# Performance work log

Measured on AMD Instinct MI355X. Metric: run time of the kernel, lower is better.

The kernel has to match this reference:

```python
import jax, jax.numpy as jnp
import numpy as np

SEQ, B, I, H = 2048, 64, 512, 512


def setup_inputs() -> dict:
    key = jax.random.key(0)
    ks = jax.random.split(key, 5)
    s = 1.0 / np.sqrt(H)  # torch.nn.RNN init scale
    return {
        "x": jax.random.normal(ks[0], (SEQ, B, I), dtype=jnp.float32),
        "W_ih": jax.random.normal(ks[1], (H, I), dtype=jnp.float32) * s,
        "W_hh": jax.random.normal(ks[2], (H, H), dtype=jnp.float32) * s,
        "b_ih": jax.random.normal(ks[3], (H,), dtype=jnp.float32) * s,
        "b_hh": jax.random.normal(ks[4], (H,), dtype=jnp.float32) * s,
    }


def reference(x, W_ih, W_hh, b_ih, b_hh):
    # Precompute input projection for all timesteps in one big GEMM: [T,B,H]
    xw = jnp.einsum("tbi,hi->tbh", x, W_ih) + b_ih + b_hh

    def step(h, xt):
        # h: [B,H]; xt: [B,H] (already includes x_t W_ih^T + biases)
        h = jnp.tanh(xt + h @ W_hh.T)
        return h, h

    h0 = jnp.zeros((x.shape[1], W_hh.shape[0]), dtype=x.dtype)
    _, out = jax.lax.scan(step, h0, xw)  # out: [T,B,H]
    return out.reshape(-1, W_hh.shape[0])  # [T*B, H], matches out.view(-1, hidden)
```

## Files before the change

### kernel.cpp

```cpp
#include <hip/hip_runtime.h>
#include <cmath>


#define SEQ_T 2048
#define BATCH 64
#define KDIM 512
#define HDIM 512

typedef __fp16 h2v __attribute__((ext_vector_type(2)));
typedef __fp16 f16x8 __attribute__((ext_vector_type(8)));
typedef float f32x4 __attribute__((ext_vector_type(4)));

static __device__ __forceinline__ f16x8 pk8(float4 a, float4 b) {
  h2v p0 = __builtin_amdgcn_cvt_pkrtz(a.x, a.y);
  h2v p1 = __builtin_amdgcn_cvt_pkrtz(a.z, a.w);
  h2v p2 = __builtin_amdgcn_cvt_pkrtz(b.x, b.y);
  h2v p3 = __builtin_amdgcn_cvt_pkrtz(b.z, b.w);
  f16x8 r;
  r[0] = p0[0]; r[1] = p0[1]; r[2] = p1[0]; r[3] = p1[1];
  r[4] = p2[0]; r[5] = p2[1]; r[6] = p3[0]; r[7] = p3[1];
  return r;
}

#define BM 128
#define BN 64
#define BK 32
#define LDA_T (BM + 4)
#define LDB_T (BN + 4)

__global__ __launch_bounds__(256) void xw_gemm(const float* __restrict__ x,
                                               const float* __restrict__ Wih,
                                               const float* __restrict__ bih,
                                               const float* __restrict__ bhh,
                                               float* __restrict__ out) {
  __shared__ float As[BK * LDA_T];
  __shared__ float Bs[BK * LDB_T];
  const int tid = threadIdx.x;
  const int nb = blockIdx.x & 7;
  const int mb = blockIdx.x >> 3;
  const int m0 = mb * BM;
  const int n0 = nb * BN;
  const int tx = tid & 15;
  const int ty = tid >> 4;

  float acc[8][4];
#pragma unroll
  for (int i = 0; i < 8; ++i)
#pragma unroll
    for (int j = 0; j < 4; ++j) acc[i][j] = 0.f;

  for (int k0 = 0; k0 < KDIM; k0 += BK) {
#pragma unroll
    for (int p = 0; p < 4; ++p) {
      int idx = tid + p * 256;
      int r = idx >> 3, c = idx & 7;
      float4 a = *(const float4*)(x + (size_t)(m0 + r) * KDIM + k0 + c * 4);
      As[(c * 4 + 0) * LDA_T + r] = a.x;
      As[(c * 4 + 1) * LDA_T + r] = a.y;
      As[(c * 4 + 2) * LDA_T + r] = a.z;
      As[(c * 4 + 3) * LDA_T + r] = a.w;
    }
#pragma unroll
    for (int p = 0; p < 2; ++p) {
      int idx = tid + p * 256;
      int r = idx >> 3, c = idx & 7;
      float4 bv = *(const float4*)(Wih + (size_t)(n0 + r) * KDIM + k0 + c * 4);
      Bs[(c * 4 + 0) * LDB_T + r] = bv.x;
      Bs[(c * 4 + 1) * LDB_T + r] = bv.y;
      Bs[(c * 4 + 2) * LDB_T + r] = bv.z;
      Bs[(c * 4 + 3) * LDB_T + r] = bv.w;
    }
    __syncthreads();
#pragma unroll
    for (int kk = 0; kk < BK; ++kk) {
      float4 a0 = *(const float4*)(As + kk * LDA_T + ty * 8);
      float4 a1 = *(const float4*)(As + kk * LDA_T + ty * 8 + 4);
      float4 b0 = *(const float4*)(Bs + kk * LDB_T + tx * 4);
      float am[8] = {a0.x, a0.y, a0.z, a0.w, a1.x, a1.y, a1.z, a1.w};
      float bn_[4] = {b0.x, b0.y, b0.z, b0.w};
#pragma unroll
      for (int i = 0; i < 8; ++i)
#pragma unroll
        for (int j = 0; j < 4; ++j) acc[i][j] = fmaf(am[i], bn_[j], acc[i][j]);
    }
    __syncthreads();
  }

  float4 bi = *(const float4*)(bih + n0 + tx * 4);
  float4 bh = *(const float4*)(bhh + n0 + tx * 4);
  const float b0 = bi.x + bh.x, b1 = bi.y + bh.y, b2 = bi.z + bh.z, b3 = bi.w + bh.w;
#pragma unroll
  for (int i = 0; i < 8; ++i) {
    float4 v = make_float4(acc[i][0] + b0, acc[i][1] + b1, acc[i][2] + b2, acc[i][3] + b3);
    *(float4*)(out + (size_t)(m0 + ty * 8 + i) * HDIM + n0 + tx * 4) = v;
  }
}


#define REPB(M, c) M(c,0) M(c,1) M(c,2) M(c,3) M(c,4) M(c,5) M(c,6) \
                   M(c,7) M(c,8) M(c,9) M(c,10) M(c,11) M(c,12)

#define DECLB(c, n) f16x8 bf##c##_##n;
#define LOADB(c, n)                                        \
  {                                                        \
    const float* p = wr##c + 32 * n;                       \
    bf##c##_##n = pk8(*(const float4*)p, *(const float4*)(p + 4)); \
  }
#define STOREB(c, n)                                                        \
  {                                                                         \
    const float* p = wr##c + 32 * n;                                        \
    *(f16x8*)(ldsm + ((n - 13) * 4 + c) * 8192 + (tid << 4)) =              \
        pk8(*(const float4*)p, *(const float4*)(p + 4));                    \
  }

#define MF(c, n) \
  d##c = __builtin_amdgcn_mfma_f32_16x16x32_f16(acur, bf##c##_##n, d##c, 0, 0, 0);
#define MFL(c, n)                                                           \
  {                                                                         \
    f16x8 bl = *(const f16x8*)(ldsm + ((n - 13) * 4 + c) * 8192 + (tid << 4)); \
    d##c = __builtin_amdgcn_mfma_f32_16x16x32_f16(acur, bl, d##c, 0, 0, 0); \
  }

#define CH(n, nn)                                                \
  {                                                              \
    f16x8 anx = *(const f16x8*)(hcv + 64 * (nn) + goff);         \
    MF(0, n) MF(1, n) MF(2, n) MF(3, n)                          \
    acur = anx;                                                  \
  }
#define CHL(n, nn)                                               \
  {                                                              \
    f16x8 anx = *(const f16x8*)(hcv + 64 * (nn) + goff);         \
    MFL(0, n) MFL(1, n) MFL(2, n) MFL(3, n)                      \
    acur = anx;                                                  \
  }

#define WLDS_BYTES (12 * 8192)
#define HBUF0 WLDS_BYTES
#define LDS_TOTAL (WLDS_BYTES + 3 * 1024)

__global__ __attribute__((amdgpu_flat_work_group_size(512, 512),
                          amdgpu_waves_per_eu(2, 2)))
void rnn_scan(const float* __restrict__ Whh, float* __restrict__ io) {
  extern __shared__ __align__(16) char ldsm[];
  const int tid = threadIdx.x;
  const int b = blockIdx.x;
  const int l = tid & 63;
  const int w = tid >> 6;
  const int m16 = l & 15;
  const int gh = l >> 4;
  const int goff = gh << 4;
  const int rb = w << 6;
  const int jo = rb + l;

  const float* wr0 = Whh + (size_t)(rb + 0 + m16) * KDIM + 8 * gh;
  const float* wr1 = Whh + (size_t)(rb + 16 + m16) * KDIM + 8 * gh;
  const float* wr2 = Whh + (size_t)(rb + 32 + m16) * KDIM + 8 * gh;
  const float* wr3 = Whh + (size_t)(rb + 48 + m16) * KDIM + 8 * gh;

  REPB(DECLB, 0) REPB(DECLB, 1) REPB(DECLB, 2) REPB(DECLB, 3)
  REPB(LOADB, 0) REPB(LOADB, 1) REPB(LOADB, 2) REPB(LOADB, 3)

  STOREB(0, 13) STOREB(1, 13) STOREB(2, 13) STOREB(3, 13)
  STOREB(0, 14) STOREB(1, 14) STOREB(2, 14) STOREB(3, 14)
  STOREB(0, 15) STOREB(1, 15) STOREB(2, 15) STOREB(3, 15)

  if (tid < 512) ((unsigned short*)(ldsm + HBUF0))[tid] = 0;
  __syncthreads();

  char* hcur = ldsm + HBUF0;
  char* hnxt = ldsm + HBUF0 + 1024;
  char* hthr = ldsm + HBUF0 + 2048;

  float* iorow = io + (size_t)b * HDIM;

  for (int t = 0; t < SEQ_T; ++t) {
    float uin = iorow[jo];

    const char* hcv = hcur;
    f16x8 acur = *(const f16x8*)(hcv + goff);

    f32x4 d0 = {0.f, 0.f, 0.f, 0.f};
    f32x4 d1 = {0.f, 0.f, 0.f, 0.f};
    f32x4 d2 = {0.f, 0.f, 0.f, 0.f};
    f32x4 d3 = {0.f, 0.f, 0.f, 0.f};

    CH(0, 1)  CH(1, 2)  CH(2, 3)  CH(3, 4)  CH(4, 5)  CH(5, 6)  CH(6, 7)
    CH(7, 8)  CH(8, 9)  CH(9, 10) CH(10, 11) CH(11, 12) CH(12, 13)
    CHL(13, 14) CHL(14, 15) CHL(15, 15)

    float za = (l & 16) ? d1[0] : d0[0];
    float zb = (l & 16) ? d3[0] : d2[0];
    float zs = (l & 32) ? zb : za;

    float z = uin + zs;
    float e = __expf(2.0f * z);
    float hn = 1.0f - 2.0f * __builtin_amdgcn_rcpf(e + 1.0f);
    iorow[jo] = hn;
    *(__fp16*)(hnxt + 2 * jo) = (__fp16)hn;

    char* tmp = hcur;
    hcur = hnxt; hnxt = hthr; hthr = tmp;
    iorow += (size_t)BATCH * HDIM;
    __syncthreads();
  }
}

extern "C" void kernel_launch(void* const* d_in, const int* in_sizes, int n_in,
                              void* d_out, int out_size, void* d_ws, size_t ws_size,
                              hipStream_t stream) {
  const float* x = (const float*)d_in[0];
  const float* Wih = (const float*)d_in[1];
  const float* Whh = (const float*)d_in[2];
  const float* bih = (const float*)d_in[3];
  const float* bhh = (const float*)d_in[4];
  float* out = (float*)d_out;

  (void)hipFuncSetAttribute((const void*)rnn_scan,
                            hipFuncAttributeMaxDynamicSharedMemorySize,
                            LDS_TOTAL);

  const int M = SEQ_T * BATCH;
  dim3 g1((M / BM) * (HDIM / BN));
  xw_gemm<<<g1, 256, 0, stream>>>(x, Wih, bih, bhh, out);

  rnn_scan<<<BATCH, 512, LDS_TOTAL, stream>>>(Whh, out);
}
```

Measured before the change: 3.998 ms.

## Use fp16 MFMA for input projection GEMM and shift scan weights to LDS

New measurement: 3.358 ms. -16.0%, faster.

```diff
diff --git a/kernel.cpp b/kernel.cpp
--- a/kernel.cpp
+++ b/kernel.cpp
@@ -22,83 +22,83 @@
   return r;
 }
 
-#define BM 128
-#define BN 64
-#define BK 32
-#define LDA_T (BM + 4)
-#define LDB_T (BN + 4)
+
+#define G_LDA 72
+
+#define MFM(mt, nt) \
+  d##mt##nt = __builtin_amdgcn_mfma_f32_16x16x32_f16(fa##mt, fb##nt, d##mt##nt, 0, 0, 0);
+
+#define EPI(mt, nt, bb)                                                     \
+  {                                                                         \
+    int row = m0 + wm + mt * 16 + (l >> 4) * 4;                             \
+    int col = n0 + wn + nt * 16 + (l & 15);                                 \
+    out[(size_t)(row + 0) * HDIM + col] = d##mt##nt[0] + bb;                \
+    out[(size_t)(row + 1) * HDIM + col] = d##mt##nt[1] + bb;                \
+    out[(size_t)(row + 2) * HDIM + col] = d##mt##nt[2] + bb;                \
+    out[(size_t)(row + 3) * HDIM + col] = d##mt##nt[3] + bb;                \
+  }
 
 __global__ __launch_bounds__(256) void xw_gemm(const float* __restrict__ x,
                                                const float* __restrict__ Wih,
                                                const float* __restrict__ bih,
                                                const float* __restrict__ bhh,
                                                float* __restrict__ out) {
-  __shared__ float As[BK * LDA_T];
-  __shared__ float Bs[BK * LDB_T];
+  __shared__ __fp16 At[128 * G_LDA];
+  __shared__ __fp16 Bt[64 * G_LDA];
   const int tid = threadIdx.x;
-  const int nb = blockIdx.x & 7;
-  const int mb = blockIdx.x >> 3;
-  const int m0 = mb * BM;
-  const int n0 = nb * BN;
-  const int tx = tid & 15;
-  const int ty = tid >> 4;
-
-  float acc[8][4];
-#pragma unroll
-  for (int i = 0; i < 8; ++i)
-#pragma unroll
-    for (int j = 0; j < 4; ++j) acc[i][j] = 0.f;
-
-  for (int k0 = 0; k0 < KDIM; k0 += BK) {
+  const int l = tid & 63;
+  const int w = tid >> 6;
+  const int m0 = (blockIdx.x >> 3) * 128;
+  const int n0 = (blockIdx.x & 7) * 64;
+  const int wm = (w >> 1) * 64;
+  const int wn = (w & 1) * 32;
+
+  const float bias0 = bih[n0 + wn + (l & 15)] + bhh[n0 + wn + (l & 15)];
+  const float bias1 = bih[n0 + wn + 16 + (l & 15)] + bhh[n0 + wn + 16 + (l & 15)];
+
+  f32x4 d00 = {0,0,0,0}, d01 = {0,0,0,0}, d10 = {0,0,0,0}, d11 = {0,0,0,0};
+  f32x4 d20 = {0,0,0,0}, d21 = {0,0,0,0}, d30 = {0,0,0,0}, d31 = {0,0,0,0};
+
+  for (int k0 = 0; k0 < KDIM; k0 += 64) {
+    __syncthreads();
 #pragma unroll
     for (int p = 0; p < 4; ++p) {
       int idx = tid + p * 256;
-      int r = idx >> 3, c = idx & 7;
-      float4 a = *(const float4*)(x + (size_t)(m0 + r) * KDIM + k0 + c * 4);
-      As[(c * 4 + 0) * LDA_T + r] = a.x;
-      As[(c * 4 + 1) * LDA_T + r] = a.y;
-      As[(c * 4 + 2) * LDA_T + r] = a.z;
-      As[(c * 4 + 3) * LDA_T + r] = a.w;
+      int r = idx >> 3, sg = idx & 7;
+      const float* ps = x + (size_t)(m0 + r) * KDIM + k0 + sg * 8;
+      *(f16x8*)(At + r * G_LDA + sg * 8) =
+          pk8(*(const float4*)ps, *(const float4*)(ps + 4));
     }
 #pragma unroll
     for (int p = 0; p < 2; ++p) {
       int idx = tid + p * 256;
-      int r = idx >> 3, c = idx & 7;
-      float4 bv = *(const float4*)(Wih + (size_t)(n0 + r) * KDIM + k0 + c * 4);
-      Bs[(c * 4 + 0) * LDB_T + r] = bv.x;
-      Bs[(c * 4 + 1) * LDB_T + r] = bv.y;
-      Bs[(c * 4 + 2) * LDB_T + r] = bv.z;
-      Bs[(c * 4 + 3) * LDB_T + r] = bv.w;
+      int r = idx >> 3, sg = idx & 7;
+      const float* ps = Wih + (size_t)(n0 + r) * KDIM + k0 + sg * 8;
+      *(f16x8*)(Bt + r * G_LDA + sg * 8) =
+          pk8(*(const float4*)ps, *(const float4*)(ps + 4));
     }
     __syncthreads();
 #pragma unroll
-    for (int kk = 0; kk < BK; ++kk) {
-      float4 a0 = *(const float4*)(As + kk * LDA_T + ty * 8);
-      float4 a1 = *(const float4*)(As + kk * LDA_T + ty * 8 + 4);
-      float4 b0 = *(const float4*)(Bs + kk * LDB_T + tx * 4);
-      float am[8] = {a0.x, a0.y, a0.z, a0.w, a1.x, a1.y, a1.z, a1.w};
-      float bn_[4] = {b0.x, b0.y, b0.z, b0.w};
-#pragma unroll
-      for (int i = 0; i < 8; ++i)
-#pragma unroll
-        for (int j = 0; j < 4; ++j) acc[i][j] = fmaf(am[i], bn_[j], acc[i][j]);
+    for (int kk = 0; kk < 2; ++kk) {
+      const int kc = kk * 32 + (l >> 4) * 8;
+      f16x8 fa0 = *(const f16x8*)(At + (wm + 0 * 16 + (l & 15)) * G_LDA + kc);
+      f16x8 fa1 = *(const f16x8*)(At + (wm + 1 * 16 + (l & 15)) * G_LDA + kc);
+      f16x8 fa2 = *(const f16x8*)(At + (wm + 2 * 16 + (l & 15)) * G_LDA + kc);
+      f16x8 fa3 = *(const f16x8*)(At + (wm + 3 * 16 + (l & 15)) * G_LDA + kc);
+      f16x8 fb0 = *(const f16x8*)(Bt + (wn + 0 * 16 + (l & 15)) * G_LDA + kc);
+      f16x8 fb1 = *(const f16x8*)(Bt + (wn + 1 * 16 + (l & 15)) * G_LDA + kc);
+      MFM(0, 0) MFM(1, 0) MFM(2, 0) MFM(3, 0)
+      MFM(0, 1) MFM(1, 1) MFM(2, 1) MFM(3, 1)
     }
-    __syncthreads();
-  }
-
-  float4 bi = *(const float4*)(bih + n0 + tx * 4);
-  float4 bh = *(const float4*)(bhh + n0 + tx * 4);
-  const float b0 = bi.x + bh.x, b1 = bi.y + bh.y, b2 = bi.z + bh.z, b3 = bi.w + bh.w;
-#pragma unroll
-  for (int i = 0; i < 8; ++i) {
-    float4 v = make_float4(acc[i][0] + b0, acc[i][1] + b1, acc[i][2] + b2, acc[i][3] + b3);
-    *(float4*)(out + (size_t)(m0 + ty * 8 + i) * HDIM + n0 + tx * 4) = v;
-  }
-}
-
-
-#define REPB(M, c) M(c,0) M(c,1) M(c,2) M(c,3) M(c,4) M(c,5) M(c,6) \
-                   M(c,7) M(c,8) M(c,9) M(c,10) M(c,11) M(c,12)
+  }
+
+  EPI(0, 0, bias0) EPI(1, 0, bias0) EPI(2, 0, bias0) EPI(3, 0, bias0)
+  EPI(0, 1, bias1) EPI(1, 1, bias1) EPI(2, 1, bias1) EPI(3, 1, bias1)
+}
+
+
+#define REPB(M, c) M(c,0) M(c,1) M(c,2) M(c,3) M(c,4) M(c,5) \
+                   M(c,6) M(c,7) M(c,8) M(c,9) M(c,10) M(c,11)
 
 #define DECLB(c, n) f16x8 bf##c##_##n;
 #define LOADB(c, n)                                        \
@@ -109,7 +109,7 @@
 #define STOREB(c, n)                                                        \
   {                                                                         \
     const float* p = wr##c + 32 * n;                                        \
-    *(f16x8*)(ldsm + ((n - 13) * 4 + c) * 8192 + (tid << 4)) =              \
+    *(f16x8*)(ldsm + ((n - 12) * 4 + c) * 8192 + (tid << 4)) =              \
         pk8(*(const float4*)p, *(const float4*)(p + 4));                    \
   }
 
@@ -117,7 +117,7 @@
   d##c = __builtin_amdgcn_mfma_f32_16x16x32_f16(acur, bf##c##_##n, d##c, 0, 0, 0);
 #define MFL(c, n)                                                           \
   {                                                                         \
-    f16x8 bl = *(const f16x8*)(ldsm + ((n - 13) * 4 + c) * 8192 + (tid << 4)); \
+    f16x8 bl = *(const f16x8*)(ldsm + ((n - 12) * 4 + c) * 8192 + (tid << 4)); \
     d##c = __builtin_amdgcn_mfma_f32_16x16x32_f16(acur, bl, d##c, 0, 0, 0); \
   }
 
@@ -134,7 +134,7 @@
     acur = anx;                                                  \
   }
 
-#define WLDS_BYTES (12 * 8192)
+#define WLDS_BYTES (16 * 8192)
 #define HBUF0 WLDS_BYTES
 #define LDS_TOTAL (WLDS_BYTES + 3 * 1024)
 
@@ -160,6 +160,7 @@
   REPB(DECLB, 0) REPB(DECLB, 1) REPB(DECLB, 2) REPB(DECLB, 3)
   REPB(LOADB, 0) REPB(LOADB, 1) REPB(LOADB, 2) REPB(LOADB, 3)
 
+  STOREB(0, 12) STOREB(1, 12) STOREB(2, 12) STOREB(3, 12)
   STOREB(0, 13) STOREB(1, 13) STOREB(2, 13) STOREB(3, 13)
   STOREB(0, 14) STOREB(1, 14) STOREB(2, 14) STOREB(3, 14)
   STOREB(0, 15) STOREB(1, 15) STOREB(2, 15) STOREB(3, 15)
@@ -184,9 +185,9 @@
     f32x4 d2 = {0.f, 0.f, 0.f, 0.f};
     f32x4 d3 = {0.f, 0.f, 0.f, 0.f};
 
-    CH(0, 1)  CH(1, 2)  CH(2, 3)  CH(3, 4)  CH(4, 5)  CH(5, 6)  CH(6, 7)
-    CH(7, 8)  CH(8, 9)  CH(9, 10) CH(10, 11) CH(11, 12) CH(12, 13)
-    CHL(13, 14) CHL(14, 15) CHL(15, 15)
+    CH(0, 1)  CH(1, 2)  CH(2, 3)   CH(3, 4)   CH(4, 5)   CH(5, 6)
+    CH(6, 7)  CH(7, 8)  CH(8, 9)   CH(9, 10)  CH(10, 11) CH(11, 12)
+    CHL(12, 13) CHL(13, 14) CHL(14, 15) CHL(15, 15)
 
     float za = (l & 16) ? d1[0] : d0[0];
     float zb = (l & 16) ? d3[0] : d2[0];
@@ -220,7 +221,7 @@
                             LDS_TOTAL);
 
   const int M = SEQ_T * BATCH;
-  dim3 g1((M / BM) * (HDIM / BN));
+  dim3 g1((M / 128) * (HDIM / 64));
   xw_gemm<<<g1, 256, 0, stream>>>(x, Wih, bih, bhh, out);
 
   rnn_scan<<<BATCH, 512, LDS_TOTAL, stream>>>(Whh, out);
```
